# Performance work log

Measured on AMD Instinct MI355X. Metric: run time of the kernel, lower is better.

## Reference

```python
import jax, jax.numpy as jnp
import numpy as np

E = 8        # num_experts
C = 1024     # n_emb
H = 4096     # n_emb * ff_mult
B, T = 4, 1024


def setup_inputs() -> dict:
    key = jax.random.key(0)
    k_x, k_g, k_1, k_2, k_3 = jax.random.split(key, 5)
    scale = 0.02
    return {
        "x": jax.random.normal(k_x, (B, T, C), dtype=jnp.float32),
        "Wg": jax.random.normal(k_g, (E, C), dtype=jnp.float32) * scale,   # gate: Linear(C, E), weight [E, C]
        "W1": jax.random.normal(k_1, (E, C, H), dtype=jnp.float32) * scale,  # per-expert w1 (transposed for einsum)
        "W2": jax.random.normal(k_2, (E, H, C), dtype=jnp.float32) * scale,  # per-expert w2
        "W3": jax.random.normal(k_3, (E, C, H), dtype=jnp.float32) * scale,  # per-expert w3
        "top_k": 2,
    }


def reference(x, Wg, W1, W2, W3, top_k):
    Bd, Td, Cd = x.shape
    xf = x.reshape(-1, Cd)                                   # [N, C]
    N = xf.shape[0]
    logits = jnp.einsum('nc,ec->ne', xf, Wg)                 # router logits [N, E]
    probs = jax.nn.softmax(logits.astype(jnp.float32), axis=-1)
    w, sel = jax.lax.top_k(probs, top_k)                     # [N, k]
    w = w / w.sum(axis=-1, keepdims=True)                    # renormalize over selected
    # combine weight per (token, expert): sum of normalized topk weights routed to e
    cw = jnp.zeros((N, E), jnp.float32).at[jnp.arange(N)[:, None], sel].add(w)
    # dense grouped SwiGLU over all experts; combine weights zero out unselected experts
    h1 = jnp.einsum('nc,ech->neh', xf, W1)                   # [N, E, H]
    g = jax.nn.silu(h1) * jnp.einsum('nc,ech->neh', xf, W3)  # [N, E, H]
    out = jnp.einsum('neh,ehc,ne->nc', g, W2, cw.astype(x.dtype))
    return out.reshape(Bd, Td, Cd)
```

## Files before the change

### kernel.cpp

```cpp
#include <hip/hip_runtime.h>
#include <hip/hip_bf16.h>

#define E_     8
#define C_     1024
#define H_     4096
#define N_TOK  4096
#define TOPK   2
#define NSLOT  (N_TOK*TOPK)
#define SPAD   (NSLOT+128)

#define LPAD 40

typedef __attribute__((ext_vector_type(4))) float f32x4;
typedef __attribute__((ext_vector_type(8))) short short8;

__device__ __forceinline__ unsigned short f2bf(float f) {
    return __builtin_bit_cast(unsigned short, __float2bfloat16(f));
}

__device__ __forceinline__ void gload16(const void* g, const void* l) {
    __builtin_amdgcn_global_load_lds(
        (const __attribute__((address_space(1))) unsigned int*)g,
        (__attribute__((address_space(3))) unsigned int*)l, 16, 0, 0);
}

#define WAITVM_(n) asm volatile("s_waitcnt vmcnt(" #n ")" ::: "memory")
#define WAITVM(n) WAITVM_(n)

__global__ void router_kernel(const float* __restrict__ x, const float* __restrict__ Wg,
                              int* __restrict__ sel, float* __restrict__ wts) {
    int wave = (blockIdx.x * blockDim.x + threadIdx.x) >> 6;
    int lane = threadIdx.x & 63;
    if (wave >= N_TOK) return;
    const float* xr = x + (size_t)wave * C_;
    float acc[E_];
#pragma unroll
    for (int e = 0; e < E_; ++e) acc[e] = 0.f;
    for (int c = lane; c < C_; c += 64) {
        float xv = xr[c];
#pragma unroll
        for (int e = 0; e < E_; ++e) acc[e] += xv * Wg[e * C_ + c];
    }
#pragma unroll
    for (int e = 0; e < E_; ++e) {
#pragma unroll
        for (int off = 32; off > 0; off >>= 1) acc[e] += __shfl_xor(acc[e], off);
    }
    if (lane == 0) {
        float mx = acc[0];
#pragma unroll
        for (int e = 1; e < E_; ++e) mx = fmaxf(mx, acc[e]);
        float p[E_]; float s = 0.f;
#pragma unroll
        for (int e = 0; e < E_; ++e) { p[e] = __expf(acc[e] - mx); s += p[e]; }
        float inv = 1.f / s;
#pragma unroll
        for (int e = 0; e < E_; ++e) p[e] *= inv;
        int b0 = 0; float v0 = p[0];
#pragma unroll
        for (int e = 1; e < E_; ++e) if (p[e] > v0) { v0 = p[e]; b0 = e; }
        int b1 = -1; float v1 = -1.f;
#pragma unroll
        for (int e = 0; e < E_; ++e) { if (e != b0 && p[e] > v1) { v1 = p[e]; b1 = e; } }
        float isum = 1.f / (v0 + v1);
        sel[wave*2]   = b0; sel[wave*2+1] = b1;
        wts[wave*2]   = v0 * isum; wts[wave*2+1] = v1 * isum;
    }
}

__global__ void assign_kernel(const int* __restrict__ sel, const float* __restrict__ wts,
                              int* __restrict__ counts, int* __restrict__ offsets,
                              int* __restrict__ pos_of_slot, int* __restrict__ token_of,
                              float* __restrict__ slotw) {
    __shared__ int cnt[256][E_];
    __shared__ int offs[E_];
    int t = threadIdx.x;
    const int PER = NSLOT / 256;
    int base = t * PER;
    int loc[E_];
#pragma unroll
    for (int e = 0; e < E_; ++e) loc[e] = 0;
    for (int i = 0; i < PER; ++i) loc[sel[base + i]]++;
#pragma unroll
    for (int e = 0; e < E_; ++e) cnt[t][e] = loc[e];
    __syncthreads();
    if (t < E_) {
        int run = 0;
        for (int i = 0; i < 256; ++i) { int c = cnt[i][t]; cnt[i][t] = run; run += c; }
        counts[t] = run;
    }
    __syncthreads();
    if (t == 0) {
        int s = 0;
        for (int e = 0; e < E_; ++e) { offs[e] = s; offsets[e] = s; s += counts[e]; }
    }
    __syncthreads();
    int run[E_];
#pragma unroll
    for (int e = 0; e < E_; ++e) run[e] = offs[e] + cnt[t][e];
    for (int i = 0; i < PER; ++i) {
        int s = base + i;
        int e = sel[s];
        int p = run[e]++;
        pos_of_slot[s] = p;
        token_of[p] = s >> 1;
        slotw[p] = wts[s];
    }
}

__global__ void copy_kernel(const float* __restrict__ x, const int* __restrict__ pos_of_slot,
                            unsigned short* __restrict__ Xg) {
    int slot = blockIdx.x * 4 + (threadIdx.x >> 6);
    int lane = threadIdx.x & 63;
    int pos = pos_of_slot[slot];
    int n = slot >> 1;
    const float* xr = x + (size_t)n * C_;
    unsigned short* dst = Xg + (size_t)pos * C_;
#pragma unroll
    for (int i = 0; i < 4; ++i) {
        int c0 = i * 256 + lane * 4;
        float4 v = *(const float4*)(xr + c0);
        ushort4 b;
        b.x = f2bf(v.x); b.y = f2bf(v.y); b.z = f2bf(v.z); b.w = f2bf(v.w);
        *(ushort4*)(dst + c0) = b;
    }
}

__global__ void wconv_kernel(const float* __restrict__ src, unsigned short* __restrict__ dst,
                             int R, int Cc) {
    int e = blockIdx.z;
    int c0 = blockIdx.x * 64;
    int r0 = blockIdx.y * 64;
    const float* s = src + (size_t)e * R * Cc;
    unsigned short* d = dst + (size_t)e * R * Cc;
    __shared__ unsigned short t_[64][72];
    int t = threadIdx.x;
    int tr = t >> 4, tc4 = (t & 15) * 4;
#pragma unroll
    for (int i = 0; i < 4; ++i) {
        int r = tr + i * 16;
        float4 v = *(const float4*)(s + (size_t)(r0 + r) * Cc + c0 + tc4);
        t_[r][tc4+0] = f2bf(v.x); t_[r][tc4+1] = f2bf(v.y);
        t_[r][tc4+2] = f2bf(v.z); t_[r][tc4+3] = f2bf(v.w);
    }
    __syncthreads();
    int oc = t >> 2, seg = (t & 3) * 16;
    short8 w0, w1;
#pragma unroll
    for (int j = 0; j < 8; ++j) {
        w0[j] = (short)t_[seg + j][oc];
        w1[j] = (short)t_[seg + 8 + j][oc];
    }
    unsigned short* dp = d + (size_t)(c0 + oc) * R + r0 + seg;
    *(short8*)dp = w0;
    *(short8*)(dp + 8) = w1;
}


#define G1_BM 256
#define G1_BN 128
#define G1_BK 64
#define G1_NT (C_/G1_BK)

#define G1_PHASE(F, ACCX, WN)                                                       \
  {                                                                                 \
    __builtin_amdgcn_s_barrier();                                                   \
    {                                                                               \
      int pn = (t + 1) & 1;                                                         \
      int tsrc = (t + 1 < G1_NT) ? (t + 1) : t;                                     \
      int k0n = tsrc * G1_BK;                                                       \
      if ((F) == 0 || (F) == 1) {                                                   \
        _Pragma("unroll")                                                           \
        for (int r = 0; r < 2; ++r) {                                               \
          int row = (F)*128 + r*64 + srow;                                          \
          int lch = pch ^ (row & 7);                                                \
          gload16(Ap + (size_t)row * C_ + k0n + lch*8,                              \
                  (char*)As + pn*32768 + (((F)*128 + r*64 + wid*8) << 7));          \
        }                                                                           \
      } else {                                                                      \
        const unsigned short* gsrc = ((F) == 2) ? B1p : B3p;                        \
        char* ldst = (char*)(((F) == 2) ? B1s : B3s) + pn*16384;                    \
        _Pragma("unroll")                                                           \
        for (int r = 0; r < 2; ++r) {                                               \
          int row = r*64 + srow;                                                    \
          int lch = pch ^ (row & 7);                                                \
          gload16(gsrc + (size_t)row * C_ + k0n + lch*8,                            \
                  ldst + ((r*64 + wid*8) << 7));                                    \
        }                                                                           \
      }                                                                             \
    }                                                                               \
    WAITVM(WN);                                                                     \
    __builtin_amdgcn_s_barrier();                                                   \
    __builtin_amdgcn_sched_barrier(0);                                              \
    {                                                                               \
      int p = t & 1; int ks = (F) & 1;                                              \
      const unsigned short* Ab = As + p*16384;                                      \
      const unsigned short* Bb = (((F) < 2) ? B1s : B3s) + p*8192;                  \
      short8 a[4], b[4];                                                            \
      _Pragma("unroll")                                                             \
      for (int m = 0; m < 4; ++m) {                                                 \
        int row = wm*64 + m*16 + fr;                                                \
        a[m] = *(const short8*)(Ab + row*64 + (((ks*4 + q) ^ (row & 7)) << 3));     \
      }                                                                             \
      _Pragma("unroll")                                                             \
      for (int n = 0; n < 4; ++n) {                                                 \
        int row = wn*64 + n*16 + fr;                                                \
        b[n] = *(const short8*)(Bb + row*64 + (((ks*4 + q) ^ (row & 7)) << 3));     \
      }                                                                             \
      __builtin_amdgcn_s_setprio(1);                                                \
      _Pragma("unroll")                                                             \
      for (int m = 0; m < 4; ++m)                                                   \
        _Pragma("unroll")                                                           \
        for (int n = 0; n < 4; ++n)                                                 \
          ACCX[m][n] = __builtin_amdgcn_mfma_f32_16x16x32_bf16(a[m], b[n], ACCX[m][n], 0, 0, 0); \
      __builtin_amdgcn_s_setprio(0);                                                \
    }                                                                               \
  }

__global__ __launch_bounds__(512, 2) void gemm1_f8(
        const unsigned short* __restrict__ Xg, const unsigned short* __restrict__ W1t,
        const unsigned short* __restrict__ W3t, unsigned short* __restrict__ G,
        const int* __restrict__ counts, const int* __restrict__ offsets) {
    int ct = blockIdx.x;
    int rslot = blockIdx.y;
    int e = rslot >> 5, rt = rslot & 31;
    int ne = counts[e];
    if (rt * G1_BM >= ne) return;
    int row0 = offsets[e] + rt * G1_BM;
    int n0 = ct * G1_BN;

    extern __shared__ unsigned short lds[];
    unsigned short* As  = lds;
    unsigned short* B1s = lds + 2*256*64;
    unsigned short* B3s = B1s + 2*128*64;

    int tid = threadIdx.x, lane = tid & 63, wid = tid >> 6;
    int wm = wid >> 1, wn = wid & 1;
    int fr = lane & 15, q = lane >> 4;
    int srow = wid * 8 + (lane >> 3);
    int pch  = lane & 7;

    const unsigned short* Ap  = Xg + (size_t)row0 * C_;
    const unsigned short* B1p = W1t + ((size_t)e * H_ + n0) * C_;
    const unsigned short* B3p = W3t + ((size_t)e * H_ + n0) * C_;

    f32x4 acc1[4][4], acc3[4][4];
#pragma unroll
    for (int m = 0; m < 4; ++m)
#pragma unroll
        for (int n = 0; n < 4; ++n) {
            acc1[m][n] = (f32x4){0.f,0.f,0.f,0.f};
            acc3[m][n] = (f32x4){0.f,0.f,0.f,0.f};
        }

#pragma unroll
    for (int u = 0; u < 2; ++u)
#pragma unroll
        for (int r = 0; r < 2; ++r) {
            int row = u*128 + r*64 + srow;
            int lch = pch ^ (row & 7);
            gload16(Ap + (size_t)row * C_ + lch*8,
                    (char*)As + ((u*128 + r*64 + wid*8) << 7));
        }
#pragma unroll
    for (int r = 0; r < 2; ++r) {
        int row = r*64 + srow;
        int lch = pch ^ (row & 7);
        gload16(B1p + (size_t)row * C_ + lch*8, (char*)B1s + ((r*64 + wid*8) << 7));
    }
#pragma unroll
    for (int r = 0; r < 2; ++r) {
        int row = r*64 + srow;
        int lch = pch ^ (row & 7);
        gload16(B3p + (size_t)row * C_ + lch*8, (char*)B3s + ((r*64 + wid*8) << 7));
    }

    for (int t = 0; t < G1_NT; ++t) {
        G1_PHASE(0, acc1, 4)
        G1_PHASE(1, acc1, 6)
        G1_PHASE(2, acc3, 6)
        G1_PHASE(3, acc3, 8)
    }
    WAITVM(0);

    int cfr = lane & 15;
#pragma unroll
    for (int m = 0; m < 4; ++m)
#pragma unroll
        for (int rg = 0; rg < 4; ++rg) {
            int row = wm*64 + m*16 + q*4 + rg;
            if (rt * G1_BM + row < ne) {
                size_t gbase = (size_t)(row0 + row) * H_ + n0 + wn*64;
#pragma unroll
                for (int n = 0; n < 4; ++n) {
                    float h1 = acc1[m][n][rg];
                    float h3 = acc3[m][n][rg];
                    float g = h1 * h3 / (1.f + __expf(-h1));
                    G[gbase + n*16 + cfr] = f2bf(g);
                }
            }
        }
}

#define G2_BM 256
#define G2_BN 128
#define G2_BK 64
#define G2_NT (H_/G2_BK)

#define G2_PHASE(F, WN)                                                             \
  {                                                                                 \
    __builtin_amdgcn_s_barrier();                                                   \
    if ((F) < 3) {                                                                  \
      int pn = (t + 1) & 1;                                                         \
      int tsrc = (t + 1 < G2_NT) ? (t + 1) : t;                                     \
      int k0n = tsrc * G2_BK;                                                       \
      if ((F) == 0 || (F) == 1) {                                                   \
        _Pragma("unroll")                                                           \
        for (int r = 0; r < 2; ++r) {                                               \
          int row = (F)*128 + r*64 + srow;                                          \
          int lch = pch ^ (row & 7);                                                \
          gload16(Ap + (size_t)row * H_ + k0n + lch*8,                              \
                  (char*)As + pn*32768 + (((F)*128 + r*64 + wid*8) << 7));          \
        }                                                                           \
      } else {                                                                      \
        _Pragma("unroll")                                                           \
        for (int r = 0; r < 2; ++r) {                                               \
          int row = r*64 + srow;                                                    \
          int lch = pch ^ (row & 7);                                                \
          gload16(Bp + (size_t)row * H_ + k0n + lch*8,                              \
                  (char*)Bs + pn*16384 + ((r*64 + wid*8) << 7));                    \
        }                                                                           \
      }                                                                             \
    }                                                                               \
    WAITVM(WN);                                                                     \
    __builtin_amdgcn_s_barrier();                                                   \
    __builtin_amdgcn_sched_barrier(0);                                              \
    {                                                                               \
      int p = t & 1; int ks = (F) >> 1; int nh = (F) & 1;                           \
      const unsigned short* Ab = As + p*16384;                                      \
      const unsigned short* Bb = Bs + p*8192;                                       \
      short8 a[4], b[2];                                                            \
      _Pragma("unroll")                                                             \
      for (int m = 0; m < 4; ++m) {                                                 \
        int row = wm*64 + m*16 + fr;                                                \
        a[m] = *(const short8*)(Ab + row*64 + (((ks*4 + q) ^ (row & 7)) << 3));     \
      }                                                                             \
      _Pragma("unroll")                                                             \
      for (int j = 0; j < 2; ++j) {                                                 \
        int row = wn*64 + (nh*2 + j)*16 + fr;                                       \
        b[j] = *(const short8*)(Bb + row*64 + (((ks*4 + q) ^ (row & 7)) << 3));     \
      }                                                                             \
      __builtin_amdgcn_s_setprio(1);                                                \
      _Pragma("unroll")                                                             \
      for (int m = 0; m < 4; ++m)                                                   \
        _Pragma("unroll")                                                           \
        for (int j = 0; j < 2; ++j)                                                 \
          acc[m][nh*2 + j] = __builtin_amdgcn_mfma_f32_16x16x32_bf16(a[m], b[j], acc[m][nh*2 + j], 0, 0, 0); \
      __builtin_amdgcn_s_setprio(0);                                                \
    }                                                                               \
  }

__global__ __launch_bounds__(512, 2) void gemm2_f8(
        const unsigned short* __restrict__ G, const unsigned short* __restrict__ W2t,
        float* __restrict__ out, const int* __restrict__ counts,
        const int* __restrict__ offsets, const int* __restrict__ token_of,
        const float* __restrict__ slotw) {
    int ct = blockIdx.x;
    int rslot = blockIdx.y;
    int e = rslot >> 5, rt = rslot & 31;
    int ne = counts[e];
    if (rt * G2_BM >= ne) return;
    int row0 = offsets[e] + rt * G2_BM;
    int n0 = ct * G2_BN;

    extern __shared__ unsigned short lds[];
    unsigned short* As = lds;
    unsigned short* Bs = lds + 2*256*64;

    int tid = threadIdx.x, lane = tid & 63, wid = tid >> 6;
    int wm = wid >> 1, wn = wid & 1;
    int fr = lane & 15, q = lane >> 4;
    int srow = wid * 8 + (lane >> 3);
    int pch  = lane & 7;

    const unsigned short* Ap = G + (size_t)row0 * H_;
    const unsigned short* Bp = W2t + ((size_t)e * C_ + n0) * H_;

    f32x4 acc[4][4];
#pragma unroll
    for (int m = 0; m < 4; ++m)
#pragma unroll
        for (int n = 0; n < 4; ++n) acc[m][n] = (f32x4){0.f,0.f,0.f,0.f};

#pragma unroll
    for (int u = 0; u < 2; ++u)
#pragma unroll
        for (int r = 0; r < 2; ++r) {
            int row = u*128 + r*64 + srow;
            int lch = pch ^ (row & 7);
            gload16(Ap + (size_t)row * H_ + lch*8,
                    (char*)As + ((u*128 + r*64 + wid*8) << 7));
        }
#pragma unroll
    for (int r = 0; r < 2; ++r) {
        int row = r*64 + srow;
        int lch = pch ^ (row & 7);
        gload16(Bp + (size_t)row * H_ + lch*8, (char*)Bs + ((r*64 + wid*8) << 7));
    }

    for (int t = 0; t < G2_NT; ++t) {
        G2_PHASE(0, 2)
        G2_PHASE(1, 4)
        G2_PHASE(2, 6)
        G2_PHASE(3, 6)
    }
    WAITVM(0);

    int cfr = lane & 15;
#pragma unroll
    for (int m = 0; m < 4; ++m)
#pragma unroll
        for (int rg = 0; rg < 4; ++rg) {
            int row = wm*64 + m*16 + q*4 + rg;
            if (rt * G2_BM + row < ne) {
                int grow = row0 + row;
                int tok = token_of[grow];
                float w = slotw[grow];
                float* orow = out + (size_t)tok * C_ + n0 + wn*64;
#pragma unroll
                for (int n = 0; n < 4; ++n)
                    atomicAdd(orow + n*16 + cfr, acc[m][n][rg] * w);
            }
        }
}

#define BM 128
#define BN 128
#define BK 32
__global__ __launch_bounds__(256, 2) void gemm1_slow(
        const unsigned short* __restrict__ Xg, const float* __restrict__ W1,
        const float* __restrict__ W3, unsigned short* __restrict__ G,
        const int* __restrict__ counts, const int* __restrict__ offsets) {
    int ct = blockIdx.x;
    int rslot = blockIdx.y;
    int e = rslot >> 5, rt = rslot & 31;
    int ne = counts[e];
    if (rt * BM >= ne) return;
    int row0 = offsets[e] + rt * BM;
    int n0 = ct * BN;

    __shared__ unsigned short As[BM][LPAD];
    __shared__ unsigned short B1s[BN][LPAD];
    __shared__ unsigned short B3s[BN][LPAD];

    int tid = threadIdx.x;
    int lane = tid & 63, wid = tid >> 6;
    int wr = (wid >> 1) * 64, wc = (wid & 1) * 64;

    f32x4 acc1[4][4], acc3[4][4];
#pragma unroll
    for (int m = 0; m < 4; ++m)
#pragma unroll
        for (int n = 0; n < 4; ++n) {
            acc1[m][n] = (f32x4){0.f,0.f,0.f,0.f};
            acc3[m][n] = (f32x4){0.f,0.f,0.f,0.f};
        }

    const float* B1p = W1 + (size_t)e * C_ * H_ + n0;
    const float* B3p = W3 + (size_t)e * C_ * H_ + n0;
    int chunk = tid & 3, rr = tid >> 2;
    int kq = tid >> 5, n4 = tid & 31;

    for (int k0 = 0; k0 < C_; k0 += BK) {
        __syncthreads();
#pragma unroll
        for (int h = 0; h < 2; ++h) {
            int row = rr + h * 64;
            uint4 v = *(const uint4*)(Xg + (size_t)(row0 + row) * C_ + k0 + chunk * 8);
            *(uint4*)&As[row][chunk * 8] = v;
        }
        {
            float4 r0 = *(const float4*)(B1p + (size_t)(k0 + kq*4 + 0) * H_ + n4*4);
            float4 r1 = *(const float4*)(B1p + (size_t)(k0 + kq*4 + 1) * H_ + n4*4);
            float4 r2 = *(const float4*)(B1p + (size_t)(k0 + kq*4 + 2) * H_ + n4*4);
            float4 r3 = *(const float4*)(B1p + (size_t)(k0 + kq*4 + 3) * H_ + n4*4);
            ushort4 w0 = {f2bf(r0.x), f2bf(r1.x), f2bf(r2.x), f2bf(r3.x)};
            ushort4 w1 = {f2bf(r0.y), f2bf(r1.y), f2bf(r2.y), f2bf(r3.y)};
            ushort4 w2 = {f2bf(r0.z), f2bf(r1.z), f2bf(r2.z), f2bf(r3.z)};
            ushort4 w3 = {f2bf(r0.w), f2bf(r1.w), f2bf(r2.w), f2bf(r3.w)};
            *(ushort4*)&B1s[n4*4+0][kq*4] = w0;
            *(ushort4*)&B1s[n4*4+1][kq*4] = w1;
            *(ushort4*)&B1s[n4*4+2][kq*4] = w2;
            *(ushort4*)&B1s[n4*4+3][kq*4] = w3;
            r0 = *(const float4*)(B3p + (size_t)(k0 + kq*4 + 0) * H_ + n4*4);
            r1 = *(const float4*)(B3p + (size_t)(k0 + kq*4 + 1) * H_ + n4*4);
            r2 = *(const float4*)(B3p + (size_t)(k0 + kq*4 + 2) * H_ + n4*4);
            r3 = *(const float4*)(B3p + (size_t)(k0 + kq*4 + 3) * H_ + n4*4);
            w0 = (ushort4){f2bf(r0.x), f2bf(r1.x), f2bf(r2.x), f2bf(r3.x)};
            w1 = (ushort4){f2bf(r0.y), f2bf(r1.y), f2bf(r2.y), f2bf(r3.y)};
            w2 = (ushort4){f2bf(r0.z), f2bf(r1.z), f2bf(r2.z), f2bf(r3.z)};
            w3 = (ushort4){f2bf(r0.w), f2bf(r1.w), f2bf(r2.w), f2bf(r3.w)};
            *(ushort4*)&B3s[n4*4+0][kq*4] = w0;
            *(ushort4*)&B3s[n4*4+1][kq*4] = w1;
            *(ushort4*)&B3s[n4*4+2][kq*4] = w2;
            *(ushort4*)&B3s[n4*4+3][kq*4] = w3;
        }
        __syncthreads();
        int q = lane >> 4, fr = lane & 15;
        short8 a[4], b1[4], b3[4];
#pragma unroll
        for (int m = 0; m < 4; ++m) a[m] = *(const short8*)&As[wr + m*16 + fr][q*8];
#pragma unroll
        for (int n = 0; n < 4; ++n) {
            b1[n] = *(const short8*)&B1s[wc + n*16 + fr][q*8];
            b3[n] = *(const short8*)&B3s[wc + n*16 + fr][q*8];
        }
#pragma unroll
        for (int m = 0; m < 4; ++m)
#pragma unroll
            for (int n = 0; n < 4; ++n) {
                acc1[m][n] = __builtin_amdgcn_mfma_f32_16x16x32_bf16(a[m], b1[n], acc1[m][n], 0, 0, 0);
                acc3[m][n] = __builtin_amdgcn_mfma_f32_16x16x32_bf16(a[m], b3[n], acc3[m][n], 0, 0, 0);
            }
    }
    int q = lane >> 4, cfr = lane & 15;
#pragma unroll
    for (int m = 0; m < 4; ++m) {
#pragma unroll
        for (int rg = 0; rg < 4; ++rg) {
            int row = wr + m*16 + q*4 + rg;
            if (rt * BM + row < ne) {
                size_t gbase = (size_t)(row0 + row) * H_ + n0;
#pragma unroll
                for (int n = 0; n < 4; ++n) {
                    float h1 = acc1[m][n][rg];
                    float h3 = acc3[m][n][rg];
                    float g = h1 * h3 / (1.f + __expf(-h1));
                    G[gbase + wc + n*16 + cfr] = f2bf(g);
                }
            }
        }
    }
}

__global__ __launch_bounds__(256, 2) void gemm2_slow(
        const unsigned short* __restrict__ G, const float* __restrict__ W2,
        float* __restrict__ out, const int* __restrict__ counts,
        const int* __restrict__ offsets, const int* __restrict__ token_of,
        const float* __restrict__ slotw) {
    int ct = blockIdx.x;
    int rslot = blockIdx.y;
    int e = rslot >> 5, rt = rslot & 31;
    int ne = counts[e];
    if (rt * BM >= ne) return;
    int row0 = offsets[e] + rt * BM;
    int n0 = ct * BN;

    __shared__ unsigned short As[BM][LPAD];
    __shared__ unsigned short Bs[BN][LPAD];

    int tid = threadIdx.x;
    int lane = tid & 63, wid = tid >> 6;
    int wr = (wid >> 1) * 64, wc = (wid & 1) * 64;

    f32x4 acc[4][4];
#pragma unroll
    for (int m = 0; m < 4; ++m)
#pragma unroll
        for (int n = 0; n < 4; ++n) acc[m][n] = (f32x4){0.f,0.f,0.f,0.f};

    const float* Bp = W2 + (size_t)e * H_ * C_ + n0;
    int chunk = tid & 3, rr = tid >> 2;
    int kq = tid >> 5, n4 = tid & 31;

    for (int k0 = 0; k0 < H_; k0 += BK) {
        __syncthreads();
#pragma unroll
        for (int h = 0; h < 2; ++h) {
            int row = rr + h * 64;
            uint4 v = *(const uint4*)(G + (size_t)(row0 + row) * H_ + k0 + chunk * 8);
            *(uint4*)&As[row][chunk * 8] = v;
        }
        {
            float4 r0 = *(const float4*)(Bp + (size_t)(k0 + kq*4 + 0) * C_ + n4*4);
            float4 r1 = *(const float4*)(Bp + (size_t)(k0 + kq*4 + 1) * C_ + n4*4);
            float4 r2 = *(const float4*)(Bp + (size_t)(k0 + kq*4 + 2) * C_ + n4*4);
            float4 r3 = *(const float4*)(Bp + (size_t)(k0 + kq*4 + 3) * C_ + n4*4);
            ushort4 w0 = {f2bf(r0.x), f2bf(r1.x), f2bf(r2.x), f2bf(r3.x)};
            ushort4 w1 = {f2bf(r0.y), f2bf(r1.y), f2bf(r2.y), f2bf(r3.y)};
            ushort4 w2 = {f2bf(r0.z), f2bf(r1.z), f2bf(r2.z), f2bf(r3.z)};
            ushort4 w3 = {f2bf(r0.w), f2bf(r1.w), f2bf(r2.w), f2bf(r3.w)};
            *(ushort4*)&Bs[n4*4+0][kq*4] = w0;
            *(ushort4*)&Bs[n4*4+1][kq*4] = w1;
            *(ushort4*)&Bs[n4*4+2][kq*4] = w2;
            *(ushort4*)&Bs[n4*4+3][kq*4] = w3;
        }
        __syncthreads();
        int q = lane >> 4, fr = lane & 15;
        short8 a[4], b[4];
#pragma unroll
        for (int m = 0; m < 4; ++m) a[m] = *(const short8*)&As[wr + m*16 + fr][q*8];
#pragma unroll
        for (int n = 0; n < 4; ++n) b[n] = *(const short8*)&Bs[wc + n*16 + fr][q*8];
#pragma unroll
        for (int m = 0; m < 4; ++m)
#pragma unroll
            for (int n = 0; n < 4; ++n)
                acc[m][n] = __builtin_amdgcn_mfma_f32_16x16x32_bf16(a[m], b[n], acc[m][n], 0, 0, 0);
    }
    int q = lane >> 4, cfr = lane & 15;
#pragma unroll
    for (int m = 0; m < 4; ++m) {
#pragma unroll
        for (int rg = 0; rg < 4; ++rg) {
            int row = wr + m*16 + q*4 + rg;
            if (rt * BM + row < ne) {
                int grow = row0 + row;
                int tok = token_of[grow];
                float w = slotw[grow];
                float* orow = out + (size_t)tok * C_ + n0;
#pragma unroll
                for (int n = 0; n < 4; ++n)
                    atomicAdd(orow + wc + n*16 + cfr, acc[m][n][rg] * w);
            }
        }
    }
}

extern "C" void kernel_launch(void* const* d_in, const int* in_sizes, int n_in,
                              void* d_out, int out_size, void* d_ws, size_t ws_size,
                              hipStream_t stream) {
    const float* x  = (const float*)d_in[0];
    const float* Wg = (const float*)d_in[1];
    const float* W1 = (const float*)d_in[2];
    const float* W2 = (const float*)d_in[3];
    const float* W3 = (const float*)d_in[4];
    float* out = (float*)d_out;

    char* ws = (char*)d_ws;
    size_t o = 0;
    int*   sel      = (int*)(ws + o);  o += (size_t)NSLOT * 4;
    float* wts      = (float*)(ws + o); o += (size_t)NSLOT * 4;
    int*   pos      = (int*)(ws + o);  o += (size_t)NSLOT * 4;
    int*   token_of = (int*)(ws + o);  o += (size_t)NSLOT * 4;
    float* slotw    = (float*)(ws + o); o += (size_t)NSLOT * 4;
    int*   counts   = (int*)(ws + o);
    int*   offsets  = counts + E_;     o += 256;
    unsigned short* Xg = (unsigned short*)(ws + o); o += (size_t)SPAD * C_ * 2;
    unsigned short* G  = (unsigned short*)(ws + o); o += (size_t)SPAD * H_ * 2;
    size_t need_slow = o;
    unsigned short* W1t = (unsigned short*)(ws + o); o += (size_t)E_ * H_ * C_ * 2;
    unsigned short* W3t = (unsigned short*)(ws + o); o += (size_t)E_ * H_ * C_ * 2;
    unsigned short* W2t = W1t;
    size_t need_fast = o;

    hipMemsetAsync(d_out, 0, (size_t)out_size * sizeof(float), stream);
    if (ws_size < need_slow) return;

    router_kernel<<<N_TOK/4, 256, 0, stream>>>(x, Wg, sel, wts);
    assign_kernel<<<1, 256, 0, stream>>>(sel, wts, counts, offsets, pos, token_of, slotw);
    copy_kernel<<<NSLOT/4, 256, 0, stream>>>(x, pos, Xg);

    if (ws_size >= need_fast) {
        hipFuncSetAttribute((const void*)gemm1_f8, hipFuncAttributeMaxDynamicSharedMemorySize, 131072);
        hipFuncSetAttribute((const void*)gemm2_f8, hipFuncAttributeMaxDynamicSharedMemorySize, 98304);
        wconv_kernel<<<dim3(H_/64, C_/64, E_), 256, 0, stream>>>(W1, W1t, C_, H_);
        wconv_kernel<<<dim3(H_/64, C_/64, E_), 256, 0, stream>>>(W3, W3t, C_, H_);
        gemm1_f8<<<dim3(H_/G1_BN, E_*32), 512, 131072, stream>>>(Xg, W1t, W3t, G, counts, offsets);
        wconv_kernel<<<dim3(C_/64, H_/64, E_), 256, 0, stream>>>(W2, W2t, H_, C_);
        gemm2_f8<<<dim3(C_/G2_BN, E_*32), 512, 98304, stream>>>(G, W2t, out, counts, offsets, token_of, slotw);
    } else {
        gemm1_slow<<<dim3(H_/BN, E_*32), 256, 0, stream>>>(Xg, W1, W3, G, counts, offsets);
        gemm2_slow<<<dim3(C_/BN, E_*32), 256, 0, stream>>>(G, W2, out, counts, offsets, token_of, slotw);
    }
}
```

Measured before the change: 487.5 us.

## Split-K the second expert GEMM with triple-buffered fragment-ordered LDS staging

Replaces the gemm2 kernel with a split-K variant that divides the H reduction into two halves, each handled by a separate block, and accumulates both into the output through the existing atomic adds. Blocks are laid out on a flat 1D grid with the expert index in the low bits. The main loop now uses BK=32 tiles in a three-stage LDS ring laid out in MFMA fragment order, which removes the XOR swizzle and the four-phase schedule. Occupancy is raised to 4 blocks per CU. The aim is more parallel blocks and better latency hiding, at the cost of twice as many atomic adds to the output and more empty early-exit blocks.

```diff
diff --git a/kernel.cpp b/kernel.cpp
--- a/kernel.cpp
+++ b/kernel.cpp
@@ -7,7 +7,7 @@
 #define N_TOK  4096
 #define TOPK   2
 #define NSLOT  (N_TOK*TOPK)
-#define SPAD   (NSLOT+128)
+#define SPAD   (NSLOT+256)
 
 #define LPAD 40
 
@@ -302,89 +302,38 @@
         }
 }
 
-#define G2_BM 256
-#define G2_BN 128
-#define G2_BK 64
-#define G2_NT (H_/G2_BK)
-
-#define G2_PHASE(F, WN)                                                             \
-  {                                                                                 \
-    __builtin_amdgcn_s_barrier();                                                   \
-    if ((F) < 3) {                                                                  \
-      int pn = (t + 1) & 1;                                                         \
-      int tsrc = (t + 1 < G2_NT) ? (t + 1) : t;                                     \
-      int k0n = tsrc * G2_BK;                                                       \
-      if ((F) == 0 || (F) == 1) {                                                   \
-        _Pragma("unroll")                                                           \
-        for (int r = 0; r < 2; ++r) {                                               \
-          int row = (F)*128 + r*64 + srow;                                          \
-          int lch = pch ^ (row & 7);                                                \
-          gload16(Ap + (size_t)row * H_ + k0n + lch*8,                              \
-                  (char*)As + pn*32768 + (((F)*128 + r*64 + wid*8) << 7));          \
-        }                                                                           \
-      } else {                                                                      \
-        _Pragma("unroll")                                                           \
-        for (int r = 0; r < 2; ++r) {                                               \
-          int row = r*64 + srow;                                                    \
-          int lch = pch ^ (row & 7);                                                \
-          gload16(Bp + (size_t)row * H_ + k0n + lch*8,                              \
-                  (char*)Bs + pn*16384 + ((r*64 + wid*8) << 7));                    \
-        }                                                                           \
-      }                                                                             \
-    }                                                                               \
-    WAITVM(WN);                                                                     \
-    __builtin_amdgcn_s_barrier();                                                   \
-    __builtin_amdgcn_sched_barrier(0);                                              \
-    {                                                                               \
-      int p = t & 1; int ks = (F) >> 1; int nh = (F) & 1;                           \
-      const unsigned short* Ab = As + p*16384;                                      \
-      const unsigned short* Bb = Bs + p*8192;                                       \
-      short8 a[4], b[2];                                                            \
-      _Pragma("unroll")                                                             \
-      for (int m = 0; m < 4; ++m) {                                                 \
-        int row = wm*64 + m*16 + fr;                                                \
-        a[m] = *(const short8*)(Ab + row*64 + (((ks*4 + q) ^ (row & 7)) << 3));     \
-      }                                                                             \
-      _Pragma("unroll")                                                             \
-      for (int j = 0; j < 2; ++j) {                                                 \
-        int row = wn*64 + (nh*2 + j)*16 + fr;                                       \
-        b[j] = *(const short8*)(Bb + row*64 + (((ks*4 + q) ^ (row & 7)) << 3));     \
-      }                                                                             \
-      __builtin_amdgcn_s_setprio(1);                                                \
-      _Pragma("unroll")                                                             \
-      for (int m = 0; m < 4; ++m)                                                   \
-        _Pragma("unroll")                                                           \
-        for (int j = 0; j < 2; ++j)                                                 \
-          acc[m][nh*2 + j] = __builtin_amdgcn_mfma_f32_16x16x32_bf16(a[m], b[j], acc[m][nh*2 + j], 0, 0, 0); \
-      __builtin_amdgcn_s_setprio(0);                                                \
-    }                                                                               \
-  }
-
-__global__ __launch_bounds__(512, 2) void gemm2_f8(
+
+#define G2_KT (H_/2)
+#define G2_NT (G2_KT/32)
+
+__global__ __launch_bounds__(512, 4) void gemm2_ks(
         const unsigned short* __restrict__ G, const unsigned short* __restrict__ W2t,
         float* __restrict__ out, const int* __restrict__ counts,
         const int* __restrict__ offsets, const int* __restrict__ token_of,
         const float* __restrict__ slotw) {
-    int ct = blockIdx.x;
-    int rslot = blockIdx.y;
-    int e = rslot >> 5, rt = rslot & 31;
+    int b = blockIdx.x;
+    int e = b & 7;
+    int j = b >> 3;
+    int ksp = j & 1;
+    int ct = (j >> 1) & 7;
+    int rt = j >> 4;
     int ne = counts[e];
-    if (rt * G2_BM >= ne) return;
-    int row0 = offsets[e] + rt * G2_BM;
-    int n0 = ct * G2_BN;
-
-    extern __shared__ unsigned short lds[];
-    unsigned short* As = lds;
-    unsigned short* Bs = lds + 2*256*64;
+    if (rt * 256 >= ne) return;
+    int row0 = offsets[e] + rt * 256;
+    int n0 = ct * 128;
+    int kbase = ksp * G2_KT;
+
+    extern __shared__ char lds2[];
+    char* As = lds2;
+    char* Bs = lds2 + 49152;
 
     int tid = threadIdx.x, lane = tid & 63, wid = tid >> 6;
     int wm = wid >> 1, wn = wid & 1;
     int fr = lane & 15, q = lane >> 4;
-    int srow = wid * 8 + (lane >> 3);
-    int pch  = lane & 7;
-
-    const unsigned short* Ap = G + (size_t)row0 * H_;
-    const unsigned short* Bp = W2t + ((size_t)e * C_ + n0) * H_;
+    int arow = lane & 15, akch = lane >> 4;
+
+    const unsigned short* Ap = G + (size_t)row0 * H_ + kbase;
+    const unsigned short* Bp = W2t + ((size_t)e * C_ + n0) * H_ + kbase;
 
     f32x4 acc[4][4];
 #pragma unroll
@@ -392,44 +341,56 @@
 #pragma unroll
         for (int n = 0; n < 4; ++n) acc[m][n] = (f32x4){0.f,0.f,0.f,0.f};
 
-#pragma unroll
-    for (int u = 0; u < 2; ++u)
-#pragma unroll
-        for (int r = 0; r < 2; ++r) {
-            int row = u*128 + r*64 + srow;
-            int lch = pch ^ (row & 7);
-            gload16(Ap + (size_t)row * H_ + lch*8,
-                    (char*)As + ((u*128 + r*64 + wid*8) << 7));
-        }
-#pragma unroll
-    for (int r = 0; r < 2; ++r) {
-        int row = r*64 + srow;
-        int lch = pch ^ (row & 7);
-        gload16(Bp + (size_t)row * H_ + lch*8, (char*)Bs + ((r*64 + wid*8) << 7));
-    }
-
+    auto STAGE = [&](int ts, int buf) {
+        int k0 = ts * 32;
+#pragma unroll
+        for (int jj = 0; jj < 2; ++jj) {
+            int ab = wid * 2 + jj;
+            gload16(Ap + (size_t)(ab * 16 + arow) * H_ + k0 + akch * 8,
+                    As + buf * 16384 + ab * 1024);
+        }
+        gload16(Bp + (size_t)(wid * 16 + arow) * H_ + k0 + akch * 8,
+                Bs + buf * 8192 + wid * 1024);
+    };
+
+    STAGE(0, 0); STAGE(1, 1);
     for (int t = 0; t < G2_NT; ++t) {
-        G2_PHASE(0, 2)
-        G2_PHASE(1, 4)
-        G2_PHASE(2, 6)
-        G2_PHASE(3, 6)
+        WAITVM(3);
+        __builtin_amdgcn_s_barrier();
+        __builtin_amdgcn_sched_barrier(0);
+        int ts = (t + 2 < G2_NT) ? t + 2 : G2_NT - 1;
+        STAGE(ts, (t + 2) % 3);
+        int buf = t % 3;
+        short8 a[4], bb[4];
+#pragma unroll
+        for (int m = 0; m < 4; ++m)
+            a[m] = *(const short8*)(As + buf * 16384 + (wm * 4 + m) * 1024 + q * 256 + fr * 16);
+#pragma unroll
+        for (int n = 0; n < 4; ++n)
+            bb[n] = *(const short8*)(Bs + buf * 8192 + (wn * 4 + n) * 1024 + q * 256 + fr * 16);
+        __builtin_amdgcn_s_setprio(1);
+#pragma unroll
+        for (int m = 0; m < 4; ++m)
+#pragma unroll
+            for (int n = 0; n < 4; ++n)
+                acc[m][n] = __builtin_amdgcn_mfma_f32_16x16x32_bf16(a[m], bb[n], acc[m][n], 0, 0, 0);
+        __builtin_amdgcn_s_setprio(0);
     }
     WAITVM(0);
 
-    int cfr = lane & 15;
 #pragma unroll
     for (int m = 0; m < 4; ++m)
 #pragma unroll
         for (int rg = 0; rg < 4; ++rg) {
             int row = wm*64 + m*16 + q*4 + rg;
-            if (rt * G2_BM + row < ne) {
+            if (rt * 256 + row < ne) {
                 int grow = row0 + row;
                 int tok = token_of[grow];
                 float w = slotw[grow];
                 float* orow = out + (size_t)tok * C_ + n0 + wn*64;
 #pragma unroll
                 for (int n = 0; n < 4; ++n)
-                    atomicAdd(orow + n*16 + cfr, acc[m][n][rg] * w);
+                    atomicAdd(orow + n*16 + fr, acc[m][n][rg] * w);
             }
         }
 }
@@ -663,12 +624,12 @@
 
     if (ws_size >= need_fast) {
         hipFuncSetAttribute((const void*)gemm1_f8, hipFuncAttributeMaxDynamicSharedMemorySize, 131072);
-        hipFuncSetAttribute((const void*)gemm2_f8, hipFuncAttributeMaxDynamicSharedMemorySize, 98304);
+        hipFuncSetAttribute((const void*)gemm2_ks, hipFuncAttributeMaxDynamicSharedMemorySize, 73728);
         wconv_kernel<<<dim3(H_/64, C_/64, E_), 256, 0, stream>>>(W1, W1t, C_, H_);
         wconv_kernel<<<dim3(H_/64, C_/64, E_), 256, 0, stream>>>(W3, W3t, C_, H_);
         gemm1_f8<<<dim3(H_/G1_BN, E_*32), 512, 131072, stream>>>(Xg, W1t, W3t, G, counts, offsets);
         wconv_kernel<<<dim3(C_/64, H_/64, E_), 256, 0, stream>>>(W2, W2t, H_, C_);
-        gemm2_f8<<<dim3(C_/G2_BN, E_*32), 512, 98304, stream>>>(G, W2t, out, counts, offsets, token_of, slotw);
+        gemm2_ks<<<4096, 512, 73728, stream>>>(G, W2t, out, counts, offsets, token_of, slotw);
     } else {
         gemm1_slow<<<dim3(H_/BN, E_*32), 256, 0, stream>>>(Xg, W1, W3, G, counts, offsets);
         gemm2_slow<<<dim3(C_/BN, E_*32), 256, 0, stream>>>(G, W2, out, counts, offsets, token_of, slotw);
```

Result: no change. 495.1 us (+1.5%).
